# Kernel optimization log

Measured on AMD Instinct MI355X. Metric: run time of the kernel, lower is better.

Reference implementation:

```python
import jax, jax.numpy as jnp
import numpy as np
from jax import lax

B, C, H, W = 2, 128, 192, 192
HEADS, WS, SS = 4, 8, 4
HID = 256  # int(C * expansion=2.0)
EPS = 1e-6


def _rpe_index(ws):
    coords = np.stack(np.meshgrid(np.arange(ws), np.arange(ws), indexing='ij')).reshape(2, -1)
    rel = (coords[:, :, None] - coords[:, None, :]).transpose(1, 2, 0)
    rel[:, :, 0] += ws - 1
    rel[:, :, 1] += ws - 1
    rel[:, :, 0] *= 2 * ws - 1
    return rel.sum(-1)  # (ws^2, ws^2) int index into rpe_table

RPE_IDX = _rpe_index(WS)


def _attn_mask(hp, wp, ws, ss):
    # Swin-style shifted-window mask, built once for static (hp, wp).
    img = np.zeros((hp, wp))
    cnt = 0
    for hs in (slice(0, -ws), slice(-ws, -ss), slice(-ss, None)):
        for wsl in (slice(0, -ws), slice(-ws, -ss), slice(-ss, None)):
            img[hs, wsl] = cnt
            cnt += 1
    mw = img.reshape(hp // ws, ws, wp // ws, ws).transpose(0, 2, 1, 3).reshape(-1, ws * ws)
    am = mw[:, None, :] - mw[:, :, None]
    return np.where(am != 0, -np.inf, 0.0).astype(np.float32)

MASK = jnp.asarray(_attn_mask(H, W, WS, SS))  # (nW, T, T)


def rmsnorm(x, s, b):
    # RMSNorm2d: variance over channel dim, computed in fp32.
    var = jnp.mean(jnp.square(x.astype(jnp.float32)), axis=1, keepdims=True)
    rms = jnp.sqrt(var + EPS).astype(x.dtype)
    return s[None, :, None, None] * x / rms + b[None, :, None, None]


def conv1x1(x, w, b):
    return jnp.einsum('oc,bchw->bohw', w, x) + b[None, :, None, None]


def dwconv3x3(x, w, b):
    y = lax.conv_general_dilated(x, w, (1, 1), 'SAME', feature_group_count=w.shape[0],
                                 dimension_numbers=('NCHW', 'OIHW', 'NCHW'))
    return y + b[None, :, None, None]


def gelu(x):
    return jax.nn.gelu(x, approximate=False)  # matches torch nn.GELU default (erf)


def conv_gated_block(x, s, b, w1, b1, wd, bd, w2, b2, beta):
    y = rmsnorm(x, s, b)
    y = conv1x1(y, w1, b1)
    y = dwconv3x3(y, wd, bd)
    u, v = jnp.split(y, 2, axis=1)
    y = conv1x1(u * gelu(v), w2, b2)
    return x + beta * y


def gated_ffn(x, s, b, w1, b1, w2, b2, gamma):
    y = rmsnorm(x, s, b)
    y = conv1x1(y, w1, b1)
    u, v = jnp.split(y, 2, axis=1)
    y = conv1x1(u * gelu(v), w2, b2)
    return x + gamma * y


def window_attention(x, qkv_w, qkv_b, rpe_table, proj_w, proj_b):
    b, c, h, w = x.shape
    hd = c // HEADS
    ws, ws2 = WS, WS * WS
    # H, W chosen divisible by ws, so _pad_to_window is a no-op here.
    x = jnp.roll(x, (-SS, -SS), axis=(2, 3))
    qkv = jnp.einsum('oc,bchw->bhwo', qkv_w, x) + qkv_b  # (B,H,W,3C)
    qkv = qkv.reshape(b, h // ws, ws, w // ws, ws, 3 * c).transpose(0, 1, 3, 2, 4, 5)
    qkv = qkv.reshape(-1, ws2, 3, HEADS, hd).transpose(2, 0, 3, 1, 4)  # (3, B*nW, nh, T, hd)
    q, k, v = qkv[0], qkv[1], qkv[2]
    attn = jnp.einsum('wnqd,wnkd->wnqk', q, k) * (hd ** -0.5)
    rpe = rpe_table[RPE_IDX.reshape(-1)].reshape(ws2, ws2, HEADS).transpose(2, 0, 1)  # (nh,T,T)
    nW = (h // ws) * (w // ws)
    attn = attn.reshape(b, nW, HEADS, ws2, ws2) + rpe[None, None] + MASK[None, :, None]
    attn = jax.nn.softmax(attn, axis=-1).reshape(-1, HEADS, ws2, ws2)
    out = jnp.einsum('wnqk,wnkd->wnqd', attn, v)
    out = out.transpose(0, 2, 1, 3).reshape(-1, ws2, c)
    out = out @ proj_w.T + proj_b  # nn.Linear
    out = out.reshape(b, h // ws, w // ws, ws, ws, c).transpose(0, 1, 3, 2, 4, 5).reshape(b, h, w, c)
    out = jnp.roll(out, (SS, SS), axis=(1, 2))
    return out.transpose(0, 3, 1, 2)


def setup_inputs():
    key = jax.random.key(0)
    ks = jax.random.split(key, 10)
    f = jnp.float32

    def nrm(k, shape, std=0.02):
        return jax.random.normal(k, shape, dtype=f) * std

    return {
        'x': jax.random.normal(ks[0], (B, C, H, W), dtype=f),
        'cg_s': jnp.ones((C,), f), 'cg_b': jnp.zeros((C,), f),
        'pw1_w': nrm(ks[1], (2 * HID, C)), 'pw1_b': jnp.zeros((2 * HID,), f),
        'dw_w': nrm(ks[2], (2 * HID, 1, 3, 3)), 'dw_b': jnp.zeros((2 * HID,), f),
        'pw2_w': nrm(ks[3], (C, HID)), 'pw2_b': jnp.zeros((C,), f),
        'beta': jnp.float32(0.5),
        'at_s': jnp.ones((C,), f), 'at_b': jnp.zeros((C,), f),
        'qkv_w': nrm(ks[4], (3 * C, C)), 'qkv_b': jnp.zeros((3 * C,), f),
        'rpe_table': nrm(ks[5], ((2 * WS - 1) ** 2, HEADS)),
        'proj_w': nrm(ks[6], (C, C)), 'proj_b': jnp.zeros((C,), f),
        'alpha': jnp.float32(0.5),
        'ff_s': jnp.ones((C,), f), 'ff_b': jnp.zeros((C,), f),
        'fc1_w': nrm(ks[7], (2 * HID, C)), 'fc1_b': jnp.zeros((2 * HID,), f),
        'fc2_w': nrm(ks[8], (C, HID)), 'fc2_b': jnp.zeros((C,), f),
        'gamma': jnp.float32(0.5),
    }


def reference(x, cg_s, cg_b, pw1_w, pw1_b, dw_w, dw_b, pw2_w, pw2_b, beta,
              at_s, at_b, qkv_w, qkv_b, rpe_table, proj_w, proj_b, alpha,
              ff_s, ff_b, fc1_w, fc1_b, fc2_w, fc2_b, gamma):
    x = conv_gated_block(x, cg_s, cg_b, pw1_w, pw1_b, dw_w, dw_b, pw2_w, pw2_b, beta)
    x = x + alpha * window_attention(rmsnorm(x, at_s, at_b), qkv_w, qkv_b, rpe_table, proj_w, proj_b)
    x = gated_ffn(x, ff_s, ff_b, fc1_w, fc1_b, fc2_w, fc2_b, gamma)
    return x
```

## Files before the change

kernel.cpp:

```cpp
#include <hip/hip_runtime.h>
#include <hip/hip_bf16.h>
#include <math.h>

#define HW   36864
#define BHW  73728

typedef float f32x4 __attribute__((ext_vector_type(4)));
typedef float f32x2 __attribute__((ext_vector_type(2)));
typedef short short8 __attribute__((ext_vector_type(8)));

__device__ __forceinline__ unsigned f2bf(float f) {
    unsigned u = __float_as_uint(f);
    return (u + 0x7fffu + ((u >> 16) & 1u)) >> 16;
}
__device__ __forceinline__ float bf2f(unsigned short s) {
    return __uint_as_float(((unsigned)s) << 16);
}
__device__ __forceinline__ float gelu_fast(float x) {
    float y = 1.5957691216057308f * fmaf(0.044715f * x * x, x, x);
    return x / (1.0f + __expf(-y));
}

__global__ __launch_bounds__(256)
void wconv_kernel(const float* __restrict__ w1, const float* __restrict__ w2,
                  const float* __restrict__ wq, const float* __restrict__ wp,
                  const float* __restrict__ wf1, const float* __restrict__ wf2,
                  const float* __restrict__ dww, const float* __restrict__ fb1,
                  ushort* __restrict__ o1, ushort* __restrict__ o2, ushort* __restrict__ oq,
                  ushort* __restrict__ op, ushort* __restrict__ of1, ushort* __restrict__ of2,
                  float* __restrict__ dwt, float* __restrict__ bg)
{
    int i = blockIdx.x * 256 + threadIdx.x;
    if      (i <  65536) o1 [i         ] = (ushort)f2bf(w1 [i         ]);
    else if (i <  98304) o2 [i -  65536] = (ushort)f2bf(w2 [i -  65536]);
    else if (i < 147456) oq [i -  98304] = (ushort)f2bf(wq [i -  98304]);
    else if (i < 163840) op [i - 147456] = (ushort)f2bf(wp [i - 147456]);
    else if (i < 229376) {
        int j = i - 163840;
        int col = j >> 7, k = j & 127;
        int src = ((col >> 4) & 1) * 256 + ((col >> 5) << 4) + (col & 15);
        of1[j] = (ushort)f2bf(wf1[(size_t)src * 128 + k]);
    }
    else if (i < 262144) of2[i - 229376] = (ushort)f2bf(wf2[i - 229376]);
    else if (i < 266752) {
        int j = i - 262144;
        int tap = j >> 9, c = j & 511;
        dwt[j] = dww[c * 9 + tap];
    }
    else if (i < 267264) {
        int j = i - 266752;
        bg[j] = fb1[((j >> 4) & 1) * 256 + ((j >> 5) << 4) + (j & 15)];
    }
}

__global__ __launch_bounds__(256)
void rmsnorm_t_kernel(const float* __restrict__ src, const float* __restrict__ s,
                      const float* __restrict__ bi, __hip_bfloat16* __restrict__ dst)
{
    __shared__ float sPar[4][64];
    __shared__ float sInv[64];
    int t = threadIdx.x, lane = t & 63, wv = t >> 6;
    int P = blockIdx.x * 64 + lane;
    int b = P / HW, pp = P - b * HW;
    const float* xb = src + (size_t)b * 128 * HW + pp;
    float v[32];
    float ss = 0.f;
#pragma unroll
    for (int i = 0; i < 32; ++i) {
        float x = xb[(size_t)(wv * 32 + i) * HW];
        v[i] = x;
        ss = fmaf(x, x, ss);
    }
    sPar[wv][lane] = ss;
    __syncthreads();
    if (t < 64) {
        float tot = sPar[0][t] + sPar[1][t] + sPar[2][t] + sPar[3][t];
        sInv[t] = 1.0f / sqrtf(tot * 0.0078125f + 1e-6f);
    }
    __syncthreads();
    float inv = sInv[lane];
    unsigned* drow = (unsigned*)(dst + (size_t)P * 128) + wv * 16;
#pragma unroll
    for (int i = 0; i < 32; i += 2) {
        int c = wv * 32 + i;
        float v0 = fmaf(s[c]     * v[i],     inv, bi[c]);
        float v1 = fmaf(s[c + 1] * v[i + 1], inv, bi[c + 1]);
        drow[i >> 1] = f2bf(v0) | (f2bf(v1) << 16);
    }
}

template<int K, int MODE>
__global__ __launch_bounds__(256, 3)
void gemm_kernel(const __hip_bfloat16* __restrict__ Abf, const __hip_bfloat16* __restrict__ Wbf,
                 const float* __restrict__ bias, int N,
                 __hip_bfloat16* __restrict__ outb)
{
    constexpr int STEPS = K / 32;
    __shared__ __align__(16) short smem[(64 + 128) * K];
    short* sA = smem;
    short* sB = smem + 64 * K;

    const short* A = (const short*)Abf;
    const short* W = (const short*)Wbf;

    int t = threadIdx.x;
    int lane = t & 63, wv = t >> 6;
    int m0 = blockIdx.x * 64;
    int n0 = blockIdx.y * 128;
    int q = lane >> 4, r16 = lane & 15;

    {
        int lr = lane >> 2, lk = lane & 3;
#pragma unroll
        for (int st = 0; st < STEPS; ++st) {
            int rowA = wv * 16 + lr;
            int kcA = lk ^ ((rowA >> 1) & 3);
            const short* ga = A + (size_t)(m0 + rowA) * K + st * 32 + kcA * 8;
            __builtin_amdgcn_global_load_lds((const __attribute__((address_space(1))) void*)ga,
                                             (__attribute__((address_space(3))) void*)(sA + st * 2048 + wv * 512), 16, 0, 0);
#pragma unroll
            for (int i = 0; i < 2; ++i) {
                int rb = wv * 32 + i * 16;
                int rowB = rb + lr;
                int kcB = lk ^ ((rowB >> 1) & 3);
                const short* gb = W + (size_t)(n0 + rowB) * K + st * 32 + kcB * 8;
                __builtin_amdgcn_global_load_lds((const __attribute__((address_space(1))) void*)gb,
                                                 (__attribute__((address_space(3))) void*)(sB + st * 4096 + rb * 32), 16, 0, 0);
            }
        }
    }

    f32x4 acc[4][2];
#pragma unroll
    for (int nt = 0; nt < 2; ++nt) {
        float bv = bias[n0 + wv * 32 + nt * 16 + r16];
#pragma unroll
        for (int mt = 0; mt < 4; ++mt) acc[mt][nt] = (f32x4){bv, bv, bv, bv};
    }
    __syncthreads();

#pragma unroll
    for (int st = 0; st < STEPS; ++st) {
        short8 af[4], bf[2];
#pragma unroll
        for (int mt = 0; mt < 4; ++mt) {
            int r = mt * 16 + r16;
            af[mt] = *(const short8*)(sA + st * 2048 + (r * 4 + (q ^ ((r >> 1) & 3))) * 8);
        }
#pragma unroll
        for (int nt = 0; nt < 2; ++nt) {
            int r = wv * 32 + nt * 16 + r16;
            bf[nt] = *(const short8*)(sB + st * 4096 + (r * 4 + (q ^ ((r >> 1) & 3))) * 8);
        }
#pragma unroll
        for (int mt = 0; mt < 4; ++mt)
#pragma unroll
            for (int nt = 0; nt < 2; ++nt)
                acc[mt][nt] = __builtin_amdgcn_mfma_f32_16x16x32_bf16(af[mt], bf[nt], acc[mt][nt], 0, 0, 0);
    }

    if constexpr (MODE == 0) {
        ushort* ob = (ushort*)outb;
#pragma unroll
        for (int mt = 0; mt < 4; ++mt) {
            int row0 = m0 + mt * 16 + q * 4;
#pragma unroll
            for (int nt = 0; nt < 2; ++nt) {
                int col = n0 + wv * 32 + nt * 16 + r16;
#pragma unroll
                for (int rg = 0; rg < 4; ++rg)
                    ob[(size_t)(row0 + rg) * N + col] = (ushort)f2bf(acc[mt][nt][rg]);
            }
        }
    } else {
        ushort* ob = (ushort*)outb;
        int ch = (n0 >> 1) + wv * 16 + r16;
#pragma unroll
        for (int mt = 0; mt < 4; ++mt) {
            int row0 = m0 + mt * 16 + q * 4;
#pragma unroll
            for (int rg = 0; rg < 4; ++rg) {
                float g = acc[mt][0][rg] * gelu_fast(acc[mt][1][rg]);
                ob[(size_t)(row0 + rg) * 256 + ch] = (ushort)f2bf(g);
            }
        }
    }
}

template<int K, bool RMS>
__global__ __launch_bounds__(256, 3)
void gemm_n128_kernel(const __hip_bfloat16* __restrict__ Abf, const __hip_bfloat16* __restrict__ Wbf,
                      const float* __restrict__ bias,
                      const float* __restrict__ rsrc, float* __restrict__ rdst,
                      const float* __restrict__ scale,
                      const float* __restrict__ rms_s, const float* __restrict__ rms_b,
                      __hip_bfloat16* __restrict__ xn)
{
    constexpr int NH = K / 128;
    __shared__ __align__(16) char smem[49152];
    short* sA = (short*)smem;
    short* sB = sA + 8192;
    float* sEp = (float*)smem;
    float* sPar = (float*)(smem + 34816);
    float* sInv = (float*)(smem + 39168);

    const short* A = (const short*)Abf;
    const short* W = (const short*)Wbf;

    int t = threadIdx.x;
    int lane = t & 63, wv = t >> 6;
    int m0 = blockIdx.x * 64;
    int q = lane >> 4, r16 = lane & 15;

    f32x4 acc[4][2];
#pragma unroll
    for (int nt = 0; nt < 2; ++nt) {
        float bv = bias[wv * 32 + nt * 16 + r16];
#pragma unroll
        for (int mt = 0; mt < 4; ++mt) acc[mt][nt] = (f32x4){bv, bv, bv, bv};
    }

#pragma unroll
    for (int h = 0; h < NH; ++h) {
        if (h) __syncthreads();
        {
            int lr = lane >> 2, lk = lane & 3;
#pragma unroll
            for (int st = 0; st < 4; ++st) {
                int kk = h * 128 + st * 32;
                int rowA = wv * 16 + lr;
                int kcA = lk ^ ((rowA >> 1) & 3);
                const short* ga = A + (size_t)(m0 + rowA) * K + kk + kcA * 8;
                __builtin_amdgcn_global_load_lds((const __attribute__((address_space(1))) void*)ga,
                                                 (__attribute__((address_space(3))) void*)(sA + st * 2048 + wv * 512), 16, 0, 0);
#pragma unroll
                for (int i = 0; i < 2; ++i) {
                    int rb = wv * 32 + i * 16;
                    int rowB = rb + lr;
                    int kcB = lk ^ ((rowB >> 1) & 3);
                    const short* gb = W + (size_t)rowB * K + kk + kcB * 8;
                    __builtin_amdgcn_global_load_lds((const __attribute__((address_space(1))) void*)gb,
                                                     (__attribute__((address_space(3))) void*)(sB + st * 4096 + rb * 32), 16, 0, 0);
                }
            }
        }
        __syncthreads();

#pragma unroll
        for (int st = 0; st < 4; ++st) {
            short8 af[4], bf[2];
#pragma unroll
            for (int mt = 0; mt < 4; ++mt) {
                int r = mt * 16 + r16;
                af[mt] = *(const short8*)(sA + st * 2048 + (r * 4 + (q ^ ((r >> 1) & 3))) * 8);
            }
#pragma unroll
            for (int nt = 0; nt < 2; ++nt) {
                int r = wv * 32 + nt * 16 + r16;
                bf[nt] = *(const short8*)(sB + st * 4096 + (r * 4 + (q ^ ((r >> 1) & 3))) * 8);
            }
#pragma unroll
            for (int mt = 0; mt < 4; ++mt)
#pragma unroll
                for (int nt = 0; nt < 2; ++nt)
                    acc[mt][nt] = __builtin_amdgcn_mfma_f32_16x16x32_bf16(af[mt], bf[nt], acc[mt][nt], 0, 0, 0);
        }
    }
    __syncthreads();

#pragma unroll
    for (int mt = 0; mt < 4; ++mt)
#pragma unroll
        for (int nt = 0; nt < 2; ++nt) {
            int c = wv * 32 + nt * 16 + r16;
            int px = mt * 16 + q * 4;
#pragma unroll
            for (int rg = 0; rg < 4; ++rg)
                sEp[c * 68 + px + rg] = acc[mt][nt][rg];
        }
    __syncthreads();

    int c16 = t >> 4, l16 = t & 15;
    int p0 = m0 + l16 * 4;
    int b = p0 / HW, pp = p0 - b * HW;
    float sc = scale[0];
    f32x4 ov[8];
    f32x4 ps = (f32x4){0.f, 0.f, 0.f, 0.f};
#pragma unroll
    for (int i = 0; i < 8; ++i) {
        int c = c16 + i * 16;
        f32x4 v = *(const f32x4*)&sEp[c * 68 + l16 * 4];
        size_t gi = (size_t)(b * 128 + c) * HW + pp;
        f32x4 r = *(const f32x4*)&rsrc[gi];
        f32x4 o = r + sc * v;
        *(f32x4*)&rdst[gi] = o;
        if constexpr (RMS) {
            ov[i] = o;
#pragma unroll
            for (int rg = 0; rg < 4; ++rg) ps[rg] = fmaf(o[rg], o[rg], ps[rg]);
        }
    }
    if constexpr (RMS) {
#pragma unroll
        for (int rg = 0; rg < 4; ++rg) sPar[(l16 * 4 + rg) * 17 + c16] = ps[rg];
        __syncthreads();
        if (t < 64) {
            float ssum = 0.f;
#pragma unroll
            for (int j = 0; j < 16; ++j) ssum += sPar[t * 17 + j];
            sInv[t] = 1.0f / sqrtf(ssum * 0.0078125f + 1e-6f);
        }
        __syncthreads();
        float iv[4];
#pragma unroll
        for (int rg = 0; rg < 4; ++rg) iv[rg] = sInv[l16 * 4 + rg];
        ushort* sXn = (ushort*)smem;
#pragma unroll
        for (int i = 0; i < 8; ++i) {
            int c = c16 + i * 16;
            float scs = rms_s[c], bcs = rms_b[c];
#pragma unroll
            for (int rg = 0; rg < 4; ++rg)
                sXn[(l16 * 4 + rg) * 132 + c] = (ushort)f2bf(fmaf(scs * ov[i][rg], iv[rg], bcs));
        }
        __syncthreads();
        {
            int px = t >> 2, qd = t & 3;
            const ushort* src = sXn + px * 132 + qd * 32;
            ushort* dst = (ushort*)xn + (size_t)(m0 + px) * 128 + qd * 32;
#pragma unroll
            for (int g = 0; g < 4; ++g)
                *(short8*)(dst + g * 8) = *(const short8*)(src + g * 8);
        }
    }
}

__global__ __launch_bounds__(256)
void dwgate_kernel(const __hip_bfloat16* __restrict__ t1, const float* __restrict__ dwt,
                   const float* __restrict__ dwb, __hip_bfloat16* __restrict__ tg)
{
    __shared__ __align__(16) char hsm[24576];
    int t = threadIdx.x;
    int tc = t & 127;
    int tp = t >> 7;
    int lane = t & 63, wvid = t >> 6;
    int bx0 = blockIdx.x;
    int bx = (bx0 & 7) * 1152 + (bx0 >> 3);
    int b = bx / 4608; int tt = bx - b * 4608;
    int th = tt / 96, tw = tt - th * 96;
    int h0 = th * 4, w = tw * 2 + tp;
    int cu = tc * 2;

    const short* t1s = (const short*)t1;
#pragma unroll
    for (int i = 0; i < 6; ++i) {
        int p = wvid * 6 + i;
        int r = p >> 2, c = p & 3;
        int hh = h0 - 1 + r, w2 = tw * 2 - 1 + c;
        char* dst = hsm + p * 1024;
        if (((unsigned)hh < 192u) & ((unsigned)w2 < 192u)) {
            const short* ga = t1s + (size_t)(b * HW + hh * 192 + w2) * 512 + lane * 8;
            __builtin_amdgcn_global_load_lds((const __attribute__((address_space(1))) void*)ga,
                                             (__attribute__((address_space(3))) void*)dst, 16, 0, 0);
        } else {
            *(f32x4*)(dst + lane * 16) = (f32x4){0.f, 0.f, 0.f, 0.f};
        }
    }

    f32x2 cwu[9], cwv[9];
#pragma unroll
    for (int tap = 0; tap < 9; ++tap) {
        cwu[tap] = *(const f32x2*)(dwt + tap * 512 + cu);
        cwv[tap] = *(const f32x2*)(dwt + tap * 512 + 256 + cu);
    }
    f32x2 bu = *(const f32x2*)(dwb + cu);
    f32x2 bv = *(const f32x2*)(dwb + 256 + cu);

    f32x2 au[4], av[4];
#pragma unroll
    for (int py = 0; py < 4; ++py) { au[py] = bu; av[py] = bv; }
    __syncthreads();

    const char* lbase = hsm + tp * 1024 + tc * 4;
#pragma unroll
    for (int r = 0; r < 6; ++r) {
#pragma unroll
        for (int dxi = 0; dxi < 3; ++dxi) {
            int off = (r * 4 + dxi) * 1024;
            uint u2 = *(const uint*)(lbase + off);
            uint v2 = *(const uint*)(lbase + off + 512);
            f32x2 uf, vf;
            uf[0] = bf2f((ushort)(u2 & 0xffffu)); uf[1] = bf2f((ushort)(u2 >> 16));
            vf[0] = bf2f((ushort)(v2 & 0xffffu)); vf[1] = bf2f((ushort)(v2 >> 16));
#pragma unroll
            for (int py = 0; py < 4; ++py) {
                int dy = r - 1 - py;
                if (dy < -1 || dy > 1) continue;
                int tap = (dy + 1) * 3 + dxi;
#pragma unroll
                for (int e = 0; e < 2; ++e) {
                    au[py][e] = fmaf(cwu[tap][e], uf[e], au[py][e]);
                    av[py][e] = fmaf(cwv[tap][e], vf[e], av[py][e]);
                }
            }
        }
    }

#pragma unroll
    for (int py = 0; py < 4; ++py) {
        uint o = f2bf(au[py][0] * gelu_fast(av[py][0]))
               | (f2bf(au[py][1] * gelu_fast(av[py][1])) << 16);
        int gp = b * HW + (h0 + py) * 192 + w;
        *(uint*)((ushort*)tg + (size_t)gp * 256 + cu) = o;
    }
}

__device__ __forceinline__ int wpix(int wh, int ww, int m) {
    int ty = m >> 3, tx = m & 7;
    int hs = wh * 8 + ty + 4; if (hs >= 192) hs -= 192;
    int wsc = ww * 8 + tx + 4; if (wsc >= 192) wsc -= 192;
    return hs * 192 + wsc;
}
__device__ __forceinline__ int wreg(int wh, int ww, int m) {
    int hr = wh * 8 + (m >> 3), wr = ww * 8 + (m & 7);
    return ((hr < 184) ? 0 : (hr < 188) ? 1 : 2) * 3 +
           ((wr < 184) ? 0 : (wr < 188) ? 1 : 2);
}

__global__ __launch_bounds__(256)
void attn_kernel(const __hip_bfloat16* __restrict__ qkv, const float* __restrict__ rpe,
                 __hip_bfloat16* __restrict__ attnout)
{
    __shared__ __align__(16) char smem[52752];
    int t = threadIdx.x;
    int lane = t & 63, head = t >> 6;
    int wh = blockIdx.x / 24, ww = blockIdx.x % 24;
    int b = blockIdx.y;
    int q = lane >> 4, r16 = lane & 15;

    float* rpe_s = (float*)(smem + 49152);
    for (int i = t; i < 900; i += 256) rpe_s[i] = rpe[i];

    char* Pbuf  = smem + head * 12288;
    char* VTbuf = Pbuf + 8192;
    const ushort* qkvu = (const ushort*)qkv;

    short8 aq[4], bk[4];
#pragma unroll
    for (int mt = 0; mt < 4; ++mt) {
        int pix = wpix(wh, ww, mt * 16 + r16);
        const ushort* rowp = qkvu + (size_t)(b * HW + pix) * 384 + head * 32 + q * 8;
        aq[mt] = *(const short8*)rowp;
        bk[mt] = *(const short8*)(rowp + 128);
    }
    {
        int pix = wpix(wh, ww, lane);
        const ushort* vp = qkvu + (size_t)(b * HW + pix) * 384 + 256 + head * 32;
        ushort* vt = (ushort*)VTbuf;
        int cpos = lane >> 3, within = lane & 7;
#pragma unroll
        for (int g = 0; g < 4; ++g) {
            short8 v8 = *(const short8*)(vp + g * 8);
#pragma unroll
            for (int e = 0; e < 8; ++e) {
                int d = g * 8 + e;
                vt[d * 64 + ((cpos ^ (d & 7)) * 8) + within] = (ushort)v8[e];
            }
        }
    }
    __syncthreads();

    f32x4 s[4][4];
#pragma unroll
    for (int mt = 0; mt < 4; ++mt)
#pragma unroll
        for (int nt = 0; nt < 4; ++nt) s[mt][nt] = (f32x4){0.f, 0.f, 0.f, 0.f};
#pragma unroll
    for (int mt = 0; mt < 4; ++mt)
#pragma unroll
        for (int nt = 0; nt < 4; ++nt)
            s[mt][nt] = __builtin_amdgcn_mfma_f32_16x16x32_bf16(aq[mt], bk[nt], s[mt][nt], 0, 0, 0);

    bool edge = (wh == 23) || (ww == 23);
    int tyj[4], txj[4], rgj[4];
#pragma unroll
    for (int nt = 0; nt < 4; ++nt) {
        int j = nt * 16 + r16;
        tyj[nt] = j >> 3; txj[nt] = j & 7;
        rgj[nt] = wreg(wh, ww, j);
    }
    float rinv[4][4];
#pragma unroll
    for (int mt = 0; mt < 4; ++mt) {
#pragma unroll
        for (int rg = 0; rg < 4; ++rg) {
            int i = mt * 16 + q * 4 + rg;
            int tyi = i >> 3, txi = i & 7;
            int rgi = edge ? wreg(wh, ww, i) : 0;
            float mx = -INFINITY;
#pragma unroll
            for (int nt = 0; nt < 4; ++nt) {
                float v = s[mt][nt][rg] * 0.17677669529663689f
                        + rpe_s[((tyi - tyj[nt] + 7) * 15 + (txi - txj[nt] + 7)) * 4 + head];
                if (edge && rgi != rgj[nt]) v = -INFINITY;
                s[mt][nt][rg] = v;
                mx = fmaxf(mx, v);
            }
            mx = fmaxf(mx, __shfl_xor(mx, 1));
            mx = fmaxf(mx, __shfl_xor(mx, 2));
            mx = fmaxf(mx, __shfl_xor(mx, 4));
            mx = fmaxf(mx, __shfl_xor(mx, 8));
            float sum = 0.f;
#pragma unroll
            for (int nt = 0; nt < 4; ++nt) {
                float e = __expf(s[mt][nt][rg] - mx);
                s[mt][nt][rg] = e;
                sum += e;
            }
            sum += __shfl_xor(sum, 1);
            sum += __shfl_xor(sum, 2);
            sum += __shfl_xor(sum, 4);
            sum += __shfl_xor(sum, 8);
            rinv[mt][rg] = 1.0f / sum;
        }
    }

    ushort* Pu = (ushort*)Pbuf;
#pragma unroll
    for (int mt = 0; mt < 4; ++mt)
#pragma unroll
        for (int rg = 0; rg < 4; ++rg) {
            int i = mt * 16 + q * 4 + rg;
            int sw = i & 7;
#pragma unroll
            for (int nt = 0; nt < 4; ++nt) {
                int j = nt * 16 + r16;
                Pu[i * 64 + ((j >> 3) ^ sw) * 8 + (j & 7)] = (ushort)f2bf(s[mt][nt][rg]);
            }
        }
    __syncthreads();

    f32x4 o[4][2];
#pragma unroll
    for (int mt = 0; mt < 4; ++mt) { o[mt][0] = (f32x4){0,0,0,0}; o[mt][1] = (f32x4){0,0,0,0}; }
    const ushort* Pus = (const ushort*)Pbuf;
    const ushort* Vus = (const ushort*)VTbuf;
#pragma unroll
    for (int ks = 0; ks < 2; ++ks) {
        int pc = ((ks * 4 + q) ^ (r16 & 7)) * 8;
        short8 ap[4];
#pragma unroll
        for (int mt = 0; mt < 4; ++mt)
            ap[mt] = *(const short8*)(Pus + (mt * 16 + r16) * 64 + pc);
        short8 bv[2];
#pragma unroll
        for (int nt = 0; nt < 2; ++nt)
            bv[nt] = *(const short8*)(Vus + (nt * 16 + r16) * 64 + pc);
#pragma unroll
        for (int mt = 0; mt < 4; ++mt)
#pragma unroll
            for (int nt = 0; nt < 2; ++nt)
                o[mt][nt] = __builtin_amdgcn_mfma_f32_16x16x32_bf16(ap[mt], bv[nt], o[mt][nt], 0, 0, 0);
    }
    __syncthreads();

    float* Of = (float*)Pbuf;
#pragma unroll
    for (int mt = 0; mt < 4; ++mt)
#pragma unroll
        for (int rg = 0; rg < 4; ++rg) {
            int i = mt * 16 + q * 4 + rg;
            int sw = i & 7;
            float sc = rinv[mt][rg];
            Of[i * 32 + (((r16 >> 2) ^ sw) * 4) + (r16 & 3)]       = o[mt][0][rg] * sc;
            Of[i * 32 + (((4 + (r16 >> 2)) ^ sw) * 4) + (r16 & 3)] = o[mt][1][rg] * sc;
        }
    __syncthreads();
    {
        int pix = wpix(wh, ww, lane);
        ushort* ob = (ushort*)attnout + (size_t)(b * HW + pix) * 128 + head * 32;
        int sw = lane & 7;
#pragma unroll
        for (int g = 0; g < 4; ++g) {
            f32x4 lo = *(const f32x4*)&Of[lane * 32 + (((g * 2) ^ sw) * 4)];
            f32x4 hi = *(const f32x4*)&Of[lane * 32 + (((g * 2 + 1) ^ sw) * 4)];
            short8 o8;
#pragma unroll
            for (int e = 0; e < 4; ++e) {
                o8[e]     = (short)(ushort)f2bf(lo[e]);
                o8[e + 4] = (short)(ushort)f2bf(hi[e]);
            }
            *(short8*)(ob + g * 8) = o8;
        }
    }
}

extern "C" void kernel_launch(void* const* d_in, const int* in_sizes, int n_in,
                              void* d_out, int out_size, void* d_ws, size_t ws_size,
                              hipStream_t stream)
{
    const float* x     = (const float*)d_in[0];
    const float* cg_s  = (const float*)d_in[1];
    const float* cg_b  = (const float*)d_in[2];
    const float* pw1_w = (const float*)d_in[3];
    const float* pw1_b = (const float*)d_in[4];
    const float* dw_w  = (const float*)d_in[5];
    const float* dw_b  = (const float*)d_in[6];
    const float* pw2_w = (const float*)d_in[7];
    const float* pw2_b = (const float*)d_in[8];
    const float* beta  = (const float*)d_in[9];
    const float* at_s  = (const float*)d_in[10];
    const float* at_b  = (const float*)d_in[11];
    const float* qkv_w = (const float*)d_in[12];
    const float* qkv_b = (const float*)d_in[13];
    const float* rpe   = (const float*)d_in[14];
    const float* proj_w= (const float*)d_in[15];
    const float* proj_b= (const float*)d_in[16];
    const float* alpha = (const float*)d_in[17];
    const float* ff_s  = (const float*)d_in[18];
    const float* ff_b  = (const float*)d_in[19];
    const float* fc1_w = (const float*)d_in[20];
    const float* fc1_b = (const float*)d_in[21];
    const float* fc2_w = (const float*)d_in[22];
    const float* fc2_b = (const float*)d_in[23];
    const float* gamma = (const float*)d_in[24];
    float* out = (float*)d_out;

    char* ws = (char*)d_ws;
    __hip_bfloat16* Xn    = (__hip_bfloat16*)ws;
    __hip_bfloat16* t1    = (__hip_bfloat16*)(ws + 18874368);
    __hip_bfloat16* qkvb  = t1;
    __hip_bfloat16* tg    = (__hip_bfloat16*)(ws + 94371840);
    __hip_bfloat16* attno = tg;
    char* wsw = ws + 132120576;
    ushort* w1b  = (ushort*)(wsw);
    ushort* w2b  = (ushort*)(wsw + 131072);
    ushort* wqb  = (ushort*)(wsw + 196608);
    ushort* wpb  = (ushort*)(wsw + 294912);
    ushort* wf1b = (ushort*)(wsw + 327680);
    ushort* wf2b = (ushort*)(wsw + 458752);
    float*  dwt  = (float*) (wsw + 524288);
    float*  bg1  = (float*) (wsw + 542720);

    wconv_kernel<<<1044, 256, 0, stream>>>(pw1_w, pw2_w, qkv_w, proj_w, fc1_w, fc2_w, dw_w, fc1_b,
                                           w1b, w2b, wqb, wpb, wf1b, wf2b, dwt, bg1);

    rmsnorm_t_kernel<<<1152, 256, 0, stream>>>(x, cg_s, cg_b, Xn);
    gemm_kernel<128, 0><<<dim3(1152, 4), 256, 0, stream>>>(Xn, (__hip_bfloat16*)w1b, pw1_b, 512, t1);
    dwgate_kernel<<<9216, 256, 0, stream>>>(t1, dwt, dw_b, tg);
    gemm_n128_kernel<256, true><<<1152, 256, 0, stream>>>(tg, (__hip_bfloat16*)w2b, pw2_b,
                                                          x, out, beta, at_s, at_b, Xn);

    gemm_kernel<128, 0><<<dim3(1152, 3), 256, 0, stream>>>(Xn, (__hip_bfloat16*)wqb, qkv_b, 384, qkvb);
    attn_kernel<<<dim3(576, 2), 256, 0, stream>>>(qkvb, rpe, attno);
    gemm_n128_kernel<128, true><<<1152, 256, 0, stream>>>(attno, (__hip_bfloat16*)wpb, proj_b,
                                                          out, out, alpha, ff_s, ff_b, Xn);

    gemm_kernel<128, 2><<<dim3(1152, 4), 256, 0, stream>>>(Xn, (__hip_bfloat16*)wf1b, bg1, 512, tg);
    gemm_n128_kernel<256, false><<<1152, 256, 0, stream>>>(tg, (__hip_bfloat16*)wf2b, fc2_b,
                                                           out, out, gamma, nullptr, nullptr, nullptr);
}
```

Before: 339.2 us.

## Halve GEMM LDS footprint with two-phase K staging and vectorise dwconv FMAs

The GEMM kernel now stages only half of K into shared memory at a time, processing K in phases of two 32-wide slices with a barrier between phases. This halves the LDS allocation, so more blocks can be resident per CU, and the explicit 3-blocks occupancy hint is removed. The cost is an extra barrier per phase and less overlap between loading and MFMA work within a block. Separately, the depthwise conv loop replaces scalar bf16 unpacking and per-element fmaf with bit-mask unpacking and packed f32x2 FMAs.

```diff
diff --git a/kernel.cpp b/kernel.cpp
--- a/kernel.cpp
+++ b/kernel.cpp
@@ -90,15 +90,16 @@
 }
 
 template<int K, int MODE>
-__global__ __launch_bounds__(256, 3)
+__global__ __launch_bounds__(256)
 void gemm_kernel(const __hip_bfloat16* __restrict__ Abf, const __hip_bfloat16* __restrict__ Wbf,
                  const float* __restrict__ bias, int N,
                  __hip_bfloat16* __restrict__ outb)
 {
     constexpr int STEPS = K / 32;
-    __shared__ __align__(16) short smem[(64 + 128) * K];
+    constexpr int PHASES = STEPS / 2;
+    __shared__ __align__(16) short smem[(64 + 128) * K / 2];
     short* sA = smem;
-    short* sB = smem + 64 * K;
+    short* sB = smem + 64 * (K / 2);
 
     const short* A = (const short*)Abf;
     const short* W = (const short*)Wbf;
@@ -108,55 +109,62 @@
     int m0 = blockIdx.x * 64;
     int n0 = blockIdx.y * 128;
     int q = lane >> 4, r16 = lane & 15;
-
-    {
-        int lr = lane >> 2, lk = lane & 3;
-#pragma unroll
-        for (int st = 0; st < STEPS; ++st) {
-            int rowA = wv * 16 + lr;
-            int kcA = lk ^ ((rowA >> 1) & 3);
-            const short* ga = A + (size_t)(m0 + rowA) * K + st * 32 + kcA * 8;
+    int lr = lane >> 2, lk = lane & 3;
+    int rowA = wv * 16 + lr;
+    int kcA = lk ^ ((rowA >> 1) & 3);
+
+    f32x4 acc[4][2];
+    bool inited = false;
+
+#pragma unroll
+    for (int ph = 0; ph < PHASES; ++ph) {
+        if (ph) __syncthreads();
+#pragma unroll
+        for (int sl = 0; sl < 2; ++sl) {
+            int gst = ph * 2 + sl;
+            const short* ga = A + (size_t)(m0 + rowA) * K + gst * 32 + kcA * 8;
             __builtin_amdgcn_global_load_lds((const __attribute__((address_space(1))) void*)ga,
-                                             (__attribute__((address_space(3))) void*)(sA + st * 2048 + wv * 512), 16, 0, 0);
+                                             (__attribute__((address_space(3))) void*)(sA + sl * 2048 + wv * 512), 16, 0, 0);
 #pragma unroll
             for (int i = 0; i < 2; ++i) {
                 int rb = wv * 32 + i * 16;
                 int rowB = rb + lr;
                 int kcB = lk ^ ((rowB >> 1) & 3);
-                const short* gb = W + (size_t)(n0 + rowB) * K + st * 32 + kcB * 8;
+                const short* gb = W + (size_t)(n0 + rowB) * K + gst * 32 + kcB * 8;
                 __builtin_amdgcn_global_load_lds((const __attribute__((address_space(1))) void*)gb,
-                                                 (__attribute__((address_space(3))) void*)(sB + st * 4096 + rb * 32), 16, 0, 0);
-            }
-        }
-    }
-
-    f32x4 acc[4][2];
-#pragma unroll
-    for (int nt = 0; nt < 2; ++nt) {
-        float bv = bias[n0 + wv * 32 + nt * 16 + r16];
-#pragma unroll
-        for (int mt = 0; mt < 4; ++mt) acc[mt][nt] = (f32x4){bv, bv, bv, bv};
-    }
-    __syncthreads();
-
-#pragma unroll
-    for (int st = 0; st < STEPS; ++st) {
-        short8 af[4], bf[2];
-#pragma unroll
-        for (int mt = 0; mt < 4; ++mt) {
-            int r = mt * 16 + r16;
-            af[mt] = *(const short8*)(sA + st * 2048 + (r * 4 + (q ^ ((r >> 1) & 3))) * 8);
-        }
-#pragma unroll
-        for (int nt = 0; nt < 2; ++nt) {
-            int r = wv * 32 + nt * 16 + r16;
-            bf[nt] = *(const short8*)(sB + st * 4096 + (r * 4 + (q ^ ((r >> 1) & 3))) * 8);
-        }
-#pragma unroll
-        for (int mt = 0; mt < 4; ++mt)
-#pragma unroll
-            for (int nt = 0; nt < 2; ++nt)
-                acc[mt][nt] = __builtin_amdgcn_mfma_f32_16x16x32_bf16(af[mt], bf[nt], acc[mt][nt], 0, 0, 0);
+                                                 (__attribute__((address_space(3))) void*)(sB + sl * 4096 + rb * 32), 16, 0, 0);
+            }
+        }
+        if (!inited) {
+            inited = true;
+#pragma unroll
+            for (int nt = 0; nt < 2; ++nt) {
+                float bv = bias[n0 + wv * 32 + nt * 16 + r16];
+#pragma unroll
+                for (int mt = 0; mt < 4; ++mt) acc[mt][nt] = (f32x4){bv, bv, bv, bv};
+            }
+        }
+        __syncthreads();
+
+#pragma unroll
+        for (int sl = 0; sl < 2; ++sl) {
+            short8 af[4], bf[2];
+#pragma unroll
+            for (int mt = 0; mt < 4; ++mt) {
+                int r = mt * 16 + r16;
+                af[mt] = *(const short8*)(sA + sl * 2048 + (r * 4 + (q ^ ((r >> 1) & 3))) * 8);
+            }
+#pragma unroll
+            for (int nt = 0; nt < 2; ++nt) {
+                int r = wv * 32 + nt * 16 + r16;
+                bf[nt] = *(const short8*)(sB + sl * 4096 + (r * 4 + (q ^ ((r >> 1) & 3))) * 8);
+            }
+#pragma unroll
+            for (int mt = 0; mt < 4; ++mt)
+#pragma unroll
+                for (int nt = 0; nt < 2; ++nt)
+                    acc[mt][nt] = __builtin_amdgcn_mfma_f32_16x16x32_bf16(af[mt], bf[nt], acc[mt][nt], 0, 0, 0);
+        }
     }
 
     if constexpr (MODE == 0) {
@@ -390,18 +398,17 @@
             uint u2 = *(const uint*)(lbase + off);
             uint v2 = *(const uint*)(lbase + off + 512);
             f32x2 uf, vf;
-            uf[0] = bf2f((ushort)(u2 & 0xffffu)); uf[1] = bf2f((ushort)(u2 >> 16));
-            vf[0] = bf2f((ushort)(v2 & 0xffffu)); vf[1] = bf2f((ushort)(v2 >> 16));
+            uf[0] = __uint_as_float(u2 << 16);
+            uf[1] = __uint_as_float(u2 & 0xffff0000u);
+            vf[0] = __uint_as_float(v2 << 16);
+            vf[1] = __uint_as_float(v2 & 0xffff0000u);
 #pragma unroll
             for (int py = 0; py < 4; ++py) {
                 int dy = r - 1 - py;
                 if (dy < -1 || dy > 1) continue;
                 int tap = (dy + 1) * 3 + dxi;
-#pragma unroll
-                for (int e = 0; e < 2; ++e) {
-                    au[py][e] = fmaf(cwu[tap][e], uf[e], au[py][e]);
-                    av[py][e] = fmaf(cwv[tap][e], vf[e], av[py][e]);
-                }
+                au[py] = __builtin_elementwise_fma(cwu[tap], uf, au[py]);
+                av[py] = __builtin_elementwise_fma(cwv[tap], vf, av[py]);
             }
         }
     }
```

Result: no change. 336.4 us (-0.8%).
